# Kernel optimization log

Measured on AMD Instinct MI355X. Metric: run time of the kernel, lower is better.

## Reference

```python
import jax, jax.numpy as jnp
import numpy as np

# Constants from TensorBase init_kwargs
AABB_MIN, AABB_MAX = -1.5, 1.5
NEAR, FAR = 2.0, 6.0
DENSITY_SHIFT = -10.0
DISTANCE_SCALE = 25.0
VIEW_PE, FEA_PE = 6, 6


def positional_encoding(x, freqs):
    # matches torch positional_encoding: interleave over freq axis, then sin/cos concat
    fb = 2.0 ** jnp.arange(freqs, dtype=x.dtype)  # [F]
    pts = (x[..., None] * fb).reshape(x.shape[:-1] + (freqs * x.shape[-1],))
    return jnp.concatenate([jnp.sin(pts), jnp.cos(pts)], axis=-1)


def trilinear_sample(vol, coords):
    """Emulates F.grid_sample(vol[None], coords, align_corners=True, padding_mode='zeros').
    vol: [C, D, H, W]; coords: [M, 3] xyz in [-1, 1] (x->W, y->H, z->D). Returns [M, C]."""
    C, D, H, W = vol.shape
    in_bounds = jnp.all((coords >= -1.0) & (coords <= 1.0), axis=-1)  # [M]
    x = jnp.clip((coords[:, 0] + 1.0) * 0.5 * (W - 1), 0.0, W - 1)
    y = jnp.clip((coords[:, 1] + 1.0) * 0.5 * (H - 1), 0.0, H - 1)
    z = jnp.clip((coords[:, 2] + 1.0) * 0.5 * (D - 1), 0.0, D - 1)
    x0 = jnp.clip(jnp.floor(x).astype(jnp.int32), 0, W - 2); x1 = x0 + 1
    y0 = jnp.clip(jnp.floor(y).astype(jnp.int32), 0, H - 2); y1 = y0 + 1
    z0 = jnp.clip(jnp.floor(z).astype(jnp.int32), 0, D - 2); z1 = z0 + 1
    fx = (x - x0)[None]; fy = (y - y0)[None]; fz = (z - z0)[None]  # [1,M]
    g = lambda zi, yi, xi: vol[:, zi, yi, xi]  # [C, M] gather
    c00 = g(z0, y0, x0) * (1 - fx) + g(z0, y0, x1) * fx
    c01 = g(z0, y1, x0) * (1 - fx) + g(z0, y1, x1) * fx
    c10 = g(z1, y0, x0) * (1 - fx) + g(z1, y0, x1) * fx
    c11 = g(z1, y1, x0) * (1 - fx) + g(z1, y1, x1) * fx
    c0 = c00 * (1 - fy) + c01 * fy
    c1 = c10 * (1 - fy) + c11 * fy
    out = c0 * (1 - fz) + c1 * fz  # [C, M]
    return (out * in_bounds[None].astype(vol.dtype)).T  # [M, C]


def setup_inputs() -> dict:
    key = jax.random.key(0)
    ks = jax.random.split(key, 10)
    N, G, APP_DIM, FC = 2048, 128, 27, 128
    in_mlpC = 2 * VIEW_PE * 3 + 2 * FEA_PE * APP_DIM + 3 + APP_DIM  # 390
    return {
        "rays_o": jax.random.normal(ks[0], (N, 3), jnp.float32) * 0.1,
        "rays_d": jax.random.normal(ks[1], (N, 3), jnp.float32),
        "density_grid": jax.random.normal(ks[2], (1, G, G, G), jnp.float32),
        "app_grid": jax.random.normal(ks[3], (APP_DIM, G, G, G), jnp.float32) * 0.1,
        "W1": jax.random.normal(ks[4], (in_mlpC, FC), jnp.float32) * (1.0 / np.sqrt(in_mlpC)),
        "b1": jnp.zeros((FC,), jnp.float32),
        "W2": jax.random.normal(ks[5], (FC, FC), jnp.float32) * (1.0 / np.sqrt(FC)),
        "b2": jnp.zeros((FC,), jnp.float32),
        "W3": jax.random.normal(ks[6], (FC, 3), jnp.float32) * (1.0 / np.sqrt(FC)),
        "b3": jnp.zeros((3,), jnp.float32),
        "n_samples": 128,
    }


def reference(rays_o, rays_d, density_grid, app_grid, W1, b1, W2, b2, W3, b3, n_samples):
    N = rays_o.shape[0]
    S = int(n_samples)
    dirs = rays_d / jnp.linalg.norm(rays_d, axis=-1, keepdims=True)
    # sample points along rays: [N, S, 3]
    t = jnp.linspace(NEAR, FAR, S, dtype=rays_o.dtype)
    pts = rays_o[:, None, :] + dirs[:, None, :] * t[None, :, None]
    # normalize_coord: (xyz - aabb[0]) * invaabbSize - 1
    norm_pts = (pts - AABB_MIN) * (2.0 / (AABB_MAX - AABB_MIN)) - 1.0
    flat = norm_pts.reshape(-1, 3)  # [N*S, 3]
    # density feature lookup + feature2density (softplus with density_shift)
    sigma_feat = trilinear_sample(density_grid, flat)[:, 0].reshape(N, S)
    sigma = jax.nn.softplus(sigma_feat + DENSITY_SHIFT)
    # raw2alpha with cumprod transmittance
    delta = (FAR - NEAR) / S
    alpha = 1.0 - jnp.exp(-sigma * delta * DISTANCE_SCALE)  # [N, S]
    T = jnp.cumprod(jnp.concatenate([jnp.ones((N, 1), alpha.dtype), 1.0 - alpha + 1e-10], axis=-1), axis=-1)
    weights = alpha * T[:, :-1]  # [N, S]
    acc = jnp.sum(weights, axis=-1)  # [N]
    # appearance feature lookup + MLPRender_Fea shading
    feats = trilinear_sample(app_grid, flat)  # [N*S, 27]
    vd = jnp.broadcast_to(dirs[:, None, :], (N, S, 3)).reshape(-1, 3)
    mlp_in = jnp.concatenate([feats, vd, positional_encoding(feats, FEA_PE), positional_encoding(vd, VIEW_PE)], axis=-1)
    h = jax.nn.relu(mlp_in @ W1 + b1)
    h = jax.nn.relu(h @ W2 + b2)
    rgb = jax.nn.sigmoid(h @ W3 + b3).reshape(N, S, 3)
    # composite with white background
    rgb_map = jnp.sum(weights[..., None] * rgb, axis=1) + (1.0 - acc)[:, None]
    return jnp.clip(rgb_map, 0.0, 1.0)
```

## Files before the change

kernel.cpp:

```cpp
#include <hip/hip_runtime.h>

#define NRAYS 2048
#define NS    128
#define G     128
#define FC    128
#define APPC  27
#define TILE  8
#define MAXP  48
#define R1    351

static __device__ __forceinline__ float tri_sample(const float* __restrict__ vol,
                                                   float gx, float gy, float gz) {
  int x0 = (int)gx; x0 = x0 < 0 ? 0 : (x0 > G - 2 ? G - 2 : x0);
  int y0 = (int)gy; y0 = y0 < 0 ? 0 : (y0 > G - 2 ? G - 2 : y0);
  int z0 = (int)gz; z0 = z0 < 0 ? 0 : (z0 > G - 2 ? G - 2 : z0);
  float fx = gx - (float)x0;
  float fy = gy - (float)y0;
  float fz = gz - (float)z0;
  const float* p = vol + ((z0 * G + y0) * G + x0);
  float v000 = p[0], v001 = p[1];
  float v010 = p[G], v011 = p[G + 1];
  const float* q = p + G * G;
  float v100 = q[0], v101 = q[1];
  float v110 = q[G], v111 = q[G + 1];
  float c00 = v000 + (v001 - v000) * fx;
  float c01 = v010 + (v011 - v010) * fx;
  float c10 = v100 + (v101 - v100) * fx;
  float c11 = v110 + (v111 - v110) * fx;
  float c0  = c00 + (c01 - c00) * fy;
  float c1  = c10 + (c11 - c10) * fy;
  return c0 + (c1 - c0) * fz;
}

static __device__ __forceinline__ float sample_alpha(const float* __restrict__ dgrid,
                                                     float ox, float oy, float oz,
                                                     float dx, float dy, float dz,
                                                     int s, bool& inb) {
  const float t  = 2.0f + (4.0f / 127.0f) * (float)s;
  const float px = (ox + dx * t) * (2.0f / 3.0f);
  const float py = (oy + dy * t) * (2.0f / 3.0f);
  const float pz = (oz + dz * t) * (2.0f / 3.0f);
  inb = (fabsf(px) <= 1.0f) && (fabsf(py) <= 1.0f) && (fabsf(pz) <= 1.0f);
  float sf = 0.0f;
  if (inb)
    sf = tri_sample(dgrid, (px + 1.0f) * 63.5f, (py + 1.0f) * 63.5f, (pz + 1.0f) * 63.5f);
  const float y  = __expf(sf - 10.0f);
  const float sp = y - 0.5f * y * y;
  return 1.0f - __expf(-sp * 0.78125f);
}

__global__ __launch_bounds__(256) void k_phase1(
    const float* __restrict__ rays_o, const float* __restrict__ rays_d,
    const float* __restrict__ dgrid,
    const float* __restrict__ W1, const float* __restrict__ W2,
    const float* __restrict__ W3, const float* __restrict__ b1,
    const float* __restrict__ b2, const float* __restrict__ b3,
    float* __restrict__ out, float* __restrict__ g_dir,
    float* __restrict__ g_woob, float* __restrict__ g_hbase,
    float* __restrict__ g_rgboob, unsigned char* __restrict__ g_cnt8,
    unsigned char* __restrict__ g_sidx, float* __restrict__ g_w) {
  const int bid = blockIdx.x;
  const int tid = threadIdx.x;

  if (bid < 512) {
    const int ray  = bid * 4 + (tid >> 6);
    const int lane = tid & 63;

    const float rdx = rays_d[ray * 3 + 0], rdy = rays_d[ray * 3 + 1], rdz = rays_d[ray * 3 + 2];
    const float inv = rsqrtf(rdx * rdx + rdy * rdy + rdz * rdz);
    const float dx = rdx * inv, dy = rdy * inv, dz = rdz * inv;
    const float ox = rays_o[ray * 3 + 0], oy = rays_o[ray * 3 + 1], oz = rays_o[ray * 3 + 2];
    if (lane == 0) {
      g_dir[ray * 3 + 0] = dx; g_dir[ray * 3 + 1] = dy; g_dir[ray * 3 + 2] = dz;
    }

    const int s0 = lane * 2, s1 = s0 + 1;
    bool in0, in1;
    const float al0 = sample_alpha(dgrid, ox, oy, oz, dx, dy, dz, s0, in0);
    const float al1 = sample_alpha(dgrid, ox, oy, oz, dx, dy, dz, s1, in1);

    const float p0 = 1.0f - al0 + 1e-10f;
    const float p1 = 1.0f - al1 + 1e-10f;
    float incl = p0 * p1;
#pragma unroll
    for (int off = 1; off < 64; off <<= 1) {
      float v = __shfl_up(incl, off);
      if (lane >= off) incl *= v;
    }
    float excl = __shfl_up(incl, 1);
    if (lane == 0) excl = 1.0f;
    const float w0 = al0 * excl;
    const float w1 = al1 * excl * p0;

    float acc  = w0 + w1;
    float woob = (in0 ? 0.0f : w0) + (in1 ? 0.0f : w1);
#pragma unroll
    for (int off = 32; off > 0; off >>= 1) {
      acc  += __shfl_xor(acc, off);
      woob += __shfl_xor(woob, off);
    }

    const unsigned long long m0 = __ballot(in0);
    const unsigned long long m1 = __ballot(in1);
    const int n_in = (int)__popcll(m0) + (int)__popcll(m1);

    if (lane == 0) {
      g_woob[ray] = woob;
      g_cnt8[ray] = (unsigned char)((n_in > MAXP) ? MAXP : n_in);
    }
    if (lane < 3) out[ray * 3 + lane] = 1.0f - acc;

    const unsigned long long low = (1ull << lane) - 1ull;
    const int r0 = (int)__popcll(m0 & low) + (int)__popcll(m1 & low);
    if (in0 && r0 < MAXP) {
      g_sidx[ray * MAXP + r0] = (unsigned char)s0;
      g_w[ray * MAXP + r0]    = w0;
    }
    if (in1) {
      const int r1 = r0 + (in0 ? 1 : 0);
      if (r1 < MAXP) {
        g_sidx[ray * MAXP + r1] = (unsigned char)s1;
        g_w[ray * MAXP + r1]    = w1;
      }
    }
    return;
  }

  __shared__ float s_in[39][8];
  __shared__ float s_h1[FC][12];
  __shared__ float s_h2[FC][12];
  __shared__ float s_bc[FC], s_ps[FC];

  const int r0 = (bid - 512) * 8;
  if (tid < 24) {
    const int j = tid & 7, d = tid >> 3;
    const float rdx = rays_d[(r0 + j) * 3 + 0], rdy = rays_d[(r0 + j) * 3 + 1],
                rdz = rays_d[(r0 + j) * 3 + 2];
    const float inv = rsqrtf(rdx * rdx + rdy * rdy + rdz * rdz);
    s_in[d][j] = (d == 0) ? rdx * inv : ((d == 1) ? rdy * inv : rdz * inv);
  }
  {
    const int nrn = tid & 127, h = tid >> 7;
    float v = 0.0f;
#pragma unroll 9
    for (int k = 192 + h; k < 354; k += 2) v += W1[k * FC + nrn];
    if (h) s_ps[nrn] = v; else s_bc[nrn] = v;
  }
  __syncthreads();
  for (int a = tid; a < 18 * 8; a += 256) {
    const int j = a & 7, idx = a >> 3, d = idx / 6, f = idx % 6;
    float sn, cs; __sincosf(s_in[d][j] * (float)(1 << f), &sn, &cs);
    s_in[3 + idx][j]  = sn;
    s_in[21 + idx][j] = cs;
  }
  __syncthreads();

  const int nrn = tid & 127;
  const int j0  = (tid >> 7) * 4;

  float a1[4];
  {
    const float bb = b1[nrn];
#pragma unroll
    for (int i = 0; i < 4; ++i) a1[i] = bb;
  }
#pragma unroll
  for (int r = 0; r < 39; ++r) {
    const int k = (r < 3) ? (27 + r) : (351 + r);
    const float wv = W1[k * FC + nrn];
    const float4 v0 = *(const float4*)&s_in[r][j0];
    a1[0] = fmaf(v0.x, wv, a1[0]); a1[1] = fmaf(v0.y, wv, a1[1]);
    a1[2] = fmaf(v0.z, wv, a1[2]); a1[3] = fmaf(v0.w, wv, a1[3]);
  }
  const float bcv = s_bc[nrn] + s_ps[nrn];
#pragma unroll
  for (int i = 0; i < 4; ++i) {
    g_hbase[(size_t)(r0 + j0 + i) * FC + nrn] = a1[i];
    s_h1[nrn][j0 + i] = fmaxf(a1[i] + bcv, 0.0f);
  }
  __syncthreads();

  float a2[4];
  {
    const float bb = b2[nrn];
#pragma unroll
    for (int i = 0; i < 4; ++i) a2[i] = bb;
  }
#pragma unroll 4
  for (int k = 0; k < FC; ++k) {
    const float wv = W2[k * FC + nrn];
    const float4 u0 = *(const float4*)&s_h1[k][j0];
    a2[0] = fmaf(u0.x, wv, a2[0]); a2[1] = fmaf(u0.y, wv, a2[1]);
    a2[2] = fmaf(u0.z, wv, a2[2]); a2[3] = fmaf(u0.w, wv, a2[3]);
  }
#pragma unroll
  for (int i = 0; i < 4; ++i) s_h2[nrn][j0 + i] = fmaxf(a2[i], 0.0f);
  __syncthreads();

  if (tid < 24) {
    const int j = tid / 3, c = tid - j * 3;
    float a3 = b3[c];
#pragma unroll 8
    for (int k = 0; k < FC; ++k)
      a3 = fmaf(s_h2[k][j], W3[k * 3 + c], a3);
    g_rgboob[(r0 + j) * 3 + c] = 1.0f / (1.0f + __expf(-a3));
  }
}

__global__ __launch_bounds__(256) void k_items(const float* __restrict__ rays_o,
                                               const float* __restrict__ g_dir,
                                               const float* __restrict__ agrid,
                                               const float* __restrict__ W1,
                                               const float* __restrict__ W2,
                                               const float* __restrict__ W3,
                                               const float* __restrict__ b2,
                                               const float* __restrict__ b3,
                                               const float* __restrict__ g_hbase,
                                               const float* __restrict__ g_woob,
                                               const float* __restrict__ g_rgboob,
                                               const unsigned char* __restrict__ g_cnt8,
                                               const unsigned char* __restrict__ g_sidx,
                                               const float* __restrict__ g_w,
                                               float* __restrict__ out) {
  const int tid = threadIdx.x;
  __shared__ int   s_pfx[NRAYS + 1];
  __shared__ int   s_wt[4];
  __shared__ float s_inT[R1][TILE];
  __shared__ float s_hT[FC][12];
  __shared__ int   s_rayid[TILE];
  __shared__ float s_jw[TILE], s_gx[TILE], s_gy[TILE], s_gz[TILE];
  __shared__ int   s_vld[TILE];

  {
    const int b0 = tid * 8;
    const uint2 cc = *(const uint2*)&g_cnt8[b0];
    int c8[8];
#pragma unroll
    for (int i = 0; i < 4; ++i) c8[i]     = (int)((cc.x >> (8 * i)) & 0xff);
#pragma unroll
    for (int i = 0; i < 4; ++i) c8[4 + i] = (int)((cc.y >> (8 * i)) & 0xff);
    int ex[8], run = 0;
#pragma unroll
    for (int i = 0; i < 8; ++i) { ex[i] = run; run += c8[i]; }
    int inclv = run;
    const int lane = tid & 63;
#pragma unroll
    for (int off = 1; off < 64; off <<= 1) {
      int v = __shfl_up(inclv, off);
      if (lane >= off) inclv += v;
    }
    if (lane == 63) s_wt[tid >> 6] = inclv;
    __syncthreads();
    int woff = 0;
    const int wq = tid >> 6;
    if (wq > 0) woff += s_wt[0];
    if (wq > 1) woff += s_wt[1];
    if (wq > 2) woff += s_wt[2];
    const int tbase = woff + inclv - run;
#pragma unroll
    for (int i = 0; i < 8; ++i) s_pfx[b0 + i] = tbase + ex[i];
    if (tid == 255) s_pfx[NRAYS] = tbase + run;
  }
  __syncthreads();
  const int total  = s_pfx[NRAYS];
  const int ntiles = 8 + ((total + TILE - 1) >> 3);

  for (int tile = blockIdx.x; tile < ntiles; tile += gridDim.x) {
    if (tile < 8) {
      const int ray = tile * 256 + tid;
      const float wv = g_woob[ray];
#pragma unroll
      for (int c = 0; c < 3; ++c)
        atomicAdd(&out[ray * 3 + c], wv * g_rgboob[ray * 3 + c]);
      continue;
    }
    const int it = tile - 8;

    if (tid < TILE) {
      const int gi  = it * TILE + tid;
      const int vld = gi < total;
      int ray = 0, s = 0;
      float wj = 0.0f;
      if (vld) {
        int lo = 0, hi = NRAYS - 1;
        while (lo < hi) {
          const int mid = (lo + hi + 1) >> 1;
          if (s_pfx[mid] <= gi) lo = mid; else hi = mid - 1;
        }
        ray = lo;
        const int slot = gi - s_pfx[ray];
        s  = g_sidx[ray * MAXP + slot];
        wj = g_w[ray * MAXP + slot];
      }
      s_rayid[tid] = ray;
      s_vld[tid]   = vld;
      s_jw[tid]    = wj;
      const float dxx = g_dir[ray * 3 + 0], dyy = g_dir[ray * 3 + 1], dzz = g_dir[ray * 3 + 2];
      const float t = 2.0f + (4.0f / 127.0f) * (float)s;
      s_gx[tid] = ((rays_o[ray * 3 + 0] + dxx * t) * (2.0f / 3.0f) + 1.0f) * 63.5f;
      s_gy[tid] = ((rays_o[ray * 3 + 1] + dyy * t) * (2.0f / 3.0f) + 1.0f) * 63.5f;
      s_gz[tid] = ((rays_o[ray * 3 + 2] + dzz * t) * (2.0f / 3.0f) + 1.0f) * 63.5f;
    }
    __syncthreads();

    if (tid < APPC * TILE) {
      const int j = tid & (TILE - 1), c = tid >> 3;
      s_inT[c][j] = s_vld[j]
                        ? tri_sample(agrid + (size_t)c * G * G * G, s_gx[j], s_gy[j], s_gz[j])
                        : 0.0f;
    }
    __syncthreads();

    for (int a = tid; a < 162 * TILE; a += 256) {
      const int j = a & (TILE - 1), idx = a >> 3;
      const int d = idx / 6, f = idx % 6;
      float sn, cs; __sincosf(s_inT[d][j] * (float)(1 << f), &sn, &cs);
      s_inT[27 + idx][j]  = sn;
      s_inT[189 + idx][j] = cs;
    }
    __syncthreads();

    const int nrn = tid & 127;
    const int j0  = (tid >> 7) * 4;

    float a1[4];
#pragma unroll
    for (int i = 0; i < 4; ++i)
      a1[i] = g_hbase[(size_t)s_rayid[j0 + i] * FC + nrn];

    const float* w1p = W1 + nrn;
#pragma unroll 9
    for (int r = 0; r < 27; ++r) {
      const float wv = w1p[r * FC];
      const float4 v0 = *(const float4*)&s_inT[r][j0];
      a1[0] = fmaf(v0.x, wv, a1[0]); a1[1] = fmaf(v0.y, wv, a1[1]);
      a1[2] = fmaf(v0.z, wv, a1[2]); a1[3] = fmaf(v0.w, wv, a1[3]);
    }
#pragma unroll 8
    for (int r = 27; r < R1; ++r) {
      const float wv = w1p[(r + 3) * FC];
      const float4 v0 = *(const float4*)&s_inT[r][j0];
      a1[0] = fmaf(v0.x, wv, a1[0]); a1[1] = fmaf(v0.y, wv, a1[1]);
      a1[2] = fmaf(v0.z, wv, a1[2]); a1[3] = fmaf(v0.w, wv, a1[3]);
    }
#pragma unroll
    for (int i = 0; i < 4; ++i) s_hT[nrn][j0 + i] = fmaxf(a1[i], 0.0f);
    __syncthreads();

    float a2[4];
    {
      const float bb = b2[nrn];
#pragma unroll
      for (int i = 0; i < 4; ++i) a2[i] = bb;
    }
#pragma unroll 4
    for (int k = 0; k < FC; ++k) {
      const float wv = W2[k * FC + nrn];
      const float4 u0 = *(const float4*)&s_hT[k][j0];
      a2[0] = fmaf(u0.x, wv, a2[0]); a2[1] = fmaf(u0.y, wv, a2[1]);
      a2[2] = fmaf(u0.z, wv, a2[2]); a2[3] = fmaf(u0.w, wv, a2[3]);
    }
    float* s_h2 = &s_inT[0][0];
#pragma unroll
    for (int i = 0; i < 4; ++i) s_h2[nrn * 12 + j0 + i] = fmaxf(a2[i], 0.0f);
    __syncthreads();

    if (tid < 3 * TILE) {
      const int j = tid / 3, c = tid - j * 3;
      if (s_vld[j] && s_jw[j] != 0.0f) {
        float a3 = b3[c];
#pragma unroll 8
        for (int k = 0; k < FC; ++k)
          a3 = fmaf(s_h2[k * 12 + j], W3[k * 3 + c], a3);
        const float rgb = 1.0f / (1.0f + __expf(-a3));
        atomicAdd(&out[s_rayid[j] * 3 + c], s_jw[j] * rgb);
      }
    }
    __syncthreads();
  }
}

extern "C" void kernel_launch(void* const* d_in, const int* in_sizes, int n_in,
                              void* d_out, int out_size, void* d_ws, size_t ws_size,
                              hipStream_t stream) {
  const float* rays_o = (const float*)d_in[0];
  const float* rays_d = (const float*)d_in[1];
  const float* dgrid  = (const float*)d_in[2];
  const float* agrid  = (const float*)d_in[3];
  const float* W1     = (const float*)d_in[4];
  const float* b1     = (const float*)d_in[5];
  const float* W2     = (const float*)d_in[6];
  const float* b2     = (const float*)d_in[7];
  const float* W3     = (const float*)d_in[8];
  const float* b3     = (const float*)d_in[9];
  float* out = (float*)d_out;

  char* ws = (char*)d_ws;
  float*         g_dir    = (float*)(ws);
  float*         g_woob   = (float*)(ws + 24576);
  float*         g_rgboob = (float*)(ws + 32768);
  unsigned char* g_cnt8   = (unsigned char*)(ws + 57344);
  float*         g_hbase  = (float*)(ws + 65536);
  float*         g_w      = (float*)(ws + 65536 + 1048576);
  unsigned char* g_sidx   = (unsigned char*)(ws + 65536 + 1048576 + 393216);

  hipLaunchKernelGGL(k_phase1, dim3(768), dim3(256), 0, stream,
                     rays_o, rays_d, dgrid, W1, W2, W3, b1, b2, b3,
                     out, g_dir, g_woob, g_hbase, g_rgboob, g_cnt8, g_sidx, g_w);
  hipLaunchKernelGGL(k_items, dim3(768), dim3(256), 0, stream,
                     rays_o, g_dir, agrid, W1, W2, W3, b2, b3,
                     g_hbase, g_woob, g_rgboob, g_cnt8, g_sidx, g_w, out);
}
```

Baseline: 58.98 us.

## Fuse out-of-bounds MLP into density kernel and drop precomputed hidden base

The density/transmittance pass now also runs the out-of-bounds MLP for its 4 rays in the same block and writes the background-plus-OOB colour directly, removing the separate OOB blocks and the atomicAdd tile loop. The item kernel no longer reads a per-ray precomputed layer-1 base from global memory. Instead it recomputes the direction and its positional encoding in idle threads and runs the full 390-row first layer. This trades 39 extra FMA rows per item and some shared memory for less global traffic, no atomics and a smaller workspace. The MLP in the prep kernel is split across two half-blocks with shared-memory reductions.

```diff
diff --git a/kernel.cpp b/kernel.cpp
--- a/kernel.cpp
+++ b/kernel.cpp
@@ -7,7 +7,7 @@
 #define APPC  27
 #define TILE  8
 #define MAXP  48
-#define R1    351
+#define NB2   768
 
 static __device__ __forceinline__ float tri_sample(const float* __restrict__ vol,
                                                    float gx, float gy, float gz) {
@@ -49,22 +49,31 @@
   return 1.0f - __expf(-sp * 0.78125f);
 }
 
-__global__ __launch_bounds__(256) void k_phase1(
+__global__ __launch_bounds__(256) void k_prep(
     const float* __restrict__ rays_o, const float* __restrict__ rays_d,
     const float* __restrict__ dgrid,
     const float* __restrict__ W1, const float* __restrict__ W2,
     const float* __restrict__ W3, const float* __restrict__ b1,
     const float* __restrict__ b2, const float* __restrict__ b3,
     float* __restrict__ out, float* __restrict__ g_dir,
-    float* __restrict__ g_woob, float* __restrict__ g_hbase,
-    float* __restrict__ g_rgboob, unsigned char* __restrict__ g_cnt8,
+    unsigned char* __restrict__ g_cnt8,
     unsigned char* __restrict__ g_sidx, float* __restrict__ g_w) {
   const int bid = blockIdx.x;
   const int tid = threadIdx.x;
 
-  if (bid < 512) {
-    const int ray  = bid * 4 + (tid >> 6);
+  __shared__ float s_dir[3][4];
+  __shared__ float s_woob[4], s_acc[4];
+  __shared__ float s_bc[FC], s_ps[FC];
+  __shared__ float s_in[39][4];
+  __shared__ float s_p[2][FC][4];
+  __shared__ float s_h1[FC][4];
+  __shared__ float s_h2[FC][4];
+  __shared__ float s_p3[12][2];
+
+  {
+    const int w    = tid >> 6;
     const int lane = tid & 63;
+    const int ray  = bid * 4 + w;
 
     const float rdx = rays_d[ray * 3 + 0], rdy = rays_d[ray * 3 + 1], rdz = rays_d[ray * 3 + 2];
     const float inv = rsqrtf(rdx * rdx + rdy * rdy + rdz * rdz);
@@ -72,6 +81,7 @@
     const float ox = rays_o[ray * 3 + 0], oy = rays_o[ray * 3 + 1], oz = rays_o[ray * 3 + 2];
     if (lane == 0) {
       g_dir[ray * 3 + 0] = dx; g_dir[ray * 3 + 1] = dy; g_dir[ray * 3 + 2] = dz;
+      s_dir[0][w] = dx; s_dir[1][w] = dy; s_dir[2][w] = dz;
     }
 
     const int s0 = lane * 2, s1 = s0 + 1;
@@ -105,10 +115,10 @@
     const int n_in = (int)__popcll(m0) + (int)__popcll(m1);
 
     if (lane == 0) {
-      g_woob[ray] = woob;
+      s_woob[w] = woob;
+      s_acc[w]  = acc;
       g_cnt8[ray] = (unsigned char)((n_in > MAXP) ? MAXP : n_in);
     }
-    if (lane < 3) out[ray * 3 + lane] = 1.0f - acc;
 
     const unsigned long long low = (1ull << lane) - 1ull;
     const int r0 = (int)__popcll(m0 & low) + (int)__popcll(m1 & low);
@@ -123,22 +133,8 @@
         g_w[ray * MAXP + r1]    = w1;
       }
     }
-    return;
-  }
-
-  __shared__ float s_in[39][8];
-  __shared__ float s_h1[FC][12];
-  __shared__ float s_h2[FC][12];
-  __shared__ float s_bc[FC], s_ps[FC];
-
-  const int r0 = (bid - 512) * 8;
-  if (tid < 24) {
-    const int j = tid & 7, d = tid >> 3;
-    const float rdx = rays_d[(r0 + j) * 3 + 0], rdy = rays_d[(r0 + j) * 3 + 1],
-                rdz = rays_d[(r0 + j) * 3 + 2];
-    const float inv = rsqrtf(rdx * rdx + rdy * rdy + rdz * rdz);
-    s_in[d][j] = (d == 0) ? rdx * inv : ((d == 1) ? rdy * inv : rdz * inv);
-  }
+  }
+
   {
     const int nrn = tid & 127, h = tid >> 7;
     float v = 0.0f;
@@ -147,63 +143,92 @@
     if (h) s_ps[nrn] = v; else s_bc[nrn] = v;
   }
   __syncthreads();
-  for (int a = tid; a < 18 * 8; a += 256) {
-    const int j = a & 7, idx = a >> 3, d = idx / 6, f = idx % 6;
-    float sn, cs; __sincosf(s_in[d][j] * (float)(1 << f), &sn, &cs);
+
+  if (tid < 12) {
+    const int j = tid & 3, d = tid >> 2;
+    s_in[d][j] = s_dir[d][j];
+  }
+  for (int a = tid; a < 72; a += 256) {
+    const int j = a & 3, idx = a >> 2, d = idx / 6, f = idx % 6;
+    float sn, cs; __sincosf(s_dir[d][j] * (float)(1 << f), &sn, &cs);
     s_in[3 + idx][j]  = sn;
     s_in[21 + idx][j] = cs;
   }
   __syncthreads();
 
   const int nrn = tid & 127;
-  const int j0  = (tid >> 7) * 4;
-
-  float a1[4];
+  const int h   = tid >> 7;
+
   {
-    const float bb = b1[nrn];
-#pragma unroll
-    for (int i = 0; i < 4; ++i) a1[i] = bb;
-  }
-#pragma unroll
-  for (int r = 0; r < 39; ++r) {
-    const int k = (r < 3) ? (27 + r) : (351 + r);
-    const float wv = W1[k * FC + nrn];
-    const float4 v0 = *(const float4*)&s_in[r][j0];
-    a1[0] = fmaf(v0.x, wv, a1[0]); a1[1] = fmaf(v0.y, wv, a1[1]);
-    a1[2] = fmaf(v0.z, wv, a1[2]); a1[3] = fmaf(v0.w, wv, a1[3]);
-  }
-  const float bcv = s_bc[nrn] + s_ps[nrn];
-#pragma unroll
-  for (int i = 0; i < 4; ++i) {
-    g_hbase[(size_t)(r0 + j0 + i) * FC + nrn] = a1[i];
-    s_h1[nrn][j0 + i] = fmaxf(a1[i] + bcv, 0.0f);
-  }
-  __syncthreads();
-
-  float a2[4];
+    float a1[4];
+    const float init = h ? (s_bc[nrn] + s_ps[nrn]) : b1[nrn];
+#pragma unroll
+    for (int i = 0; i < 4; ++i) a1[i] = h ? init : init;
+#pragma unroll
+    for (int i = 0; i < 4; ++i) a1[i] = init;
+    const int rlo = h ? 20 : 0, rhi = h ? 39 : 20;
+    for (int r = rlo; r < rhi; ++r) {
+      const int k = (r < 3) ? (27 + r) : (351 + r);
+      const float wv = W1[k * FC + nrn];
+      const float4 v0 = *(const float4*)&s_in[r][0];
+      a1[0] = fmaf(v0.x, wv, a1[0]); a1[1] = fmaf(v0.y, wv, a1[1]);
+      a1[2] = fmaf(v0.z, wv, a1[2]); a1[3] = fmaf(v0.w, wv, a1[3]);
+    }
+    *(float4*)&s_p[h][nrn][0] = make_float4(a1[0], a1[1], a1[2], a1[3]);
+  }
+  __syncthreads();
+  if (tid < FC) {
+    const float4 q0 = *(const float4*)&s_p[0][tid][0];
+    const float4 q1 = *(const float4*)&s_p[1][tid][0];
+    s_h1[tid][0] = fmaxf(q0.x + q1.x, 0.0f);
+    s_h1[tid][1] = fmaxf(q0.y + q1.y, 0.0f);
+    s_h1[tid][2] = fmaxf(q0.z + q1.z, 0.0f);
+    s_h1[tid][3] = fmaxf(q0.w + q1.w, 0.0f);
+  }
+  __syncthreads();
+
   {
-    const float bb = b2[nrn];
-#pragma unroll
-    for (int i = 0; i < 4; ++i) a2[i] = bb;
-  }
+    float a2[4] = {0.0f, 0.0f, 0.0f, 0.0f};
+    const int k0 = h * 64;
 #pragma unroll 4
-  for (int k = 0; k < FC; ++k) {
-    const float wv = W2[k * FC + nrn];
-    const float4 u0 = *(const float4*)&s_h1[k][j0];
-    a2[0] = fmaf(u0.x, wv, a2[0]); a2[1] = fmaf(u0.y, wv, a2[1]);
-    a2[2] = fmaf(u0.z, wv, a2[2]); a2[3] = fmaf(u0.w, wv, a2[3]);
-  }
-#pragma unroll
-  for (int i = 0; i < 4; ++i) s_h2[nrn][j0 + i] = fmaxf(a2[i], 0.0f);
+    for (int kk = 0; kk < 64; ++kk) {
+      const int k = k0 + kk;
+      const float wv = W2[k * FC + nrn];
+      const float4 u0 = *(const float4*)&s_h1[k][0];
+      a2[0] = fmaf(u0.x, wv, a2[0]); a2[1] = fmaf(u0.y, wv, a2[1]);
+      a2[2] = fmaf(u0.z, wv, a2[2]); a2[3] = fmaf(u0.w, wv, a2[3]);
+    }
+    *(float4*)&s_p[h][nrn][0] = make_float4(a2[0], a2[1], a2[2], a2[3]);
+  }
+  __syncthreads();
+  if (tid < FC) {
+    const float bb = b2[tid];
+    const float4 q0 = *(const float4*)&s_p[0][tid][0];
+    const float4 q1 = *(const float4*)&s_p[1][tid][0];
+    s_h2[tid][0] = fmaxf(bb + q0.x + q1.x, 0.0f);
+    s_h2[tid][1] = fmaxf(bb + q0.y + q1.y, 0.0f);
+    s_h2[tid][2] = fmaxf(bb + q0.z + q1.z, 0.0f);
+    s_h2[tid][3] = fmaxf(bb + q0.w + q1.w, 0.0f);
+  }
   __syncthreads();
 
   if (tid < 24) {
+    const int q = tid >> 1, hf = tid & 1;
+    const int j = q / 3, c = q - j * 3;
+    float a3 = 0.0f;
+#pragma unroll 8
+    for (int kk = 0; kk < 64; ++kk) {
+      const int k = hf * 64 + kk;
+      a3 = fmaf(s_h2[k][j], W3[k * 3 + c], a3);
+    }
+    s_p3[q][hf] = a3;
+  }
+  __syncthreads();
+  if (tid < 12) {
     const int j = tid / 3, c = tid - j * 3;
-    float a3 = b3[c];
-#pragma unroll 8
-    for (int k = 0; k < FC; ++k)
-      a3 = fmaf(s_h2[k][j], W3[k * 3 + c], a3);
-    g_rgboob[(r0 + j) * 3 + c] = 1.0f / (1.0f + __expf(-a3));
+    const float a3  = b3[c] + s_p3[tid][0] + s_p3[tid][1];
+    const float rgb = 1.0f / (1.0f + __expf(-a3));
+    out[(bid * 4 + j) * 3 + c] = s_woob[j] * rgb + (1.0f - s_acc[j]);
   }
 }
 
@@ -213,11 +238,9 @@
                                                const float* __restrict__ W1,
                                                const float* __restrict__ W2,
                                                const float* __restrict__ W3,
+                                               const float* __restrict__ b1,
                                                const float* __restrict__ b2,
                                                const float* __restrict__ b3,
-                                               const float* __restrict__ g_hbase,
-                                               const float* __restrict__ g_woob,
-                                               const float* __restrict__ g_rgboob,
                                                const unsigned char* __restrict__ g_cnt8,
                                                const unsigned char* __restrict__ g_sidx,
                                                const float* __restrict__ g_w,
@@ -225,7 +248,7 @@
   const int tid = threadIdx.x;
   __shared__ int   s_pfx[NRAYS + 1];
   __shared__ int   s_wt[4];
-  __shared__ float s_inT[R1][TILE];
+  __shared__ float s_inT[390][TILE];
   __shared__ float s_hT[FC][12];
   __shared__ int   s_rayid[TILE];
   __shared__ float s_jw[TILE], s_gx[TILE], s_gy[TILE], s_gz[TILE];
@@ -263,21 +286,11 @@
   }
   __syncthreads();
   const int total  = s_pfx[NRAYS];
-  const int ntiles = 8 + ((total + TILE - 1) >> 3);
-
-  for (int tile = blockIdx.x; tile < ntiles; tile += gridDim.x) {
-    if (tile < 8) {
-      const int ray = tile * 256 + tid;
-      const float wv = g_woob[ray];
-#pragma unroll
-      for (int c = 0; c < 3; ++c)
-        atomicAdd(&out[ray * 3 + c], wv * g_rgboob[ray * 3 + c]);
-      continue;
-    }
-    const int it = tile - 8;
-
+  const int ntiles = (total + TILE - 1) >> 3;
+
+  for (int tile = blockIdx.x; tile < ntiles; tile += NB2) {
     if (tid < TILE) {
-      const int gi  = it * TILE + tid;
+      const int gi  = tile * TILE + tid;
       const int vld = gi < total;
       int ray = 0, s = 0;
       float wj = 0.0f;
@@ -308,6 +321,19 @@
       s_inT[c][j] = s_vld[j]
                         ? tri_sample(agrid + (size_t)c * G * G * G, s_gx[j], s_gy[j], s_gz[j])
                         : 0.0f;
+    } else {
+      for (int a = tid - 216; a < 24; a += 40) {
+        const int j = a & 7, d = a >> 3;
+        s_inT[351 + d][j] = g_dir[s_rayid[j] * 3 + d];
+      }
+      for (int a = tid - 216; a < 144; a += 40) {
+        const int j = a & 7, idx = a >> 3;
+        const int d = idx / 6, f = idx % 6;
+        const float dv = g_dir[s_rayid[j] * 3 + d];
+        float sn, cs; __sincosf(dv * (float)(1 << f), &sn, &cs);
+        s_inT[354 + idx][j] = sn;
+        s_inT[372 + idx][j] = cs;
+      }
     }
     __syncthreads();
 
@@ -324,10 +350,11 @@
     const int j0  = (tid >> 7) * 4;
 
     float a1[4];
-#pragma unroll
-    for (int i = 0; i < 4; ++i)
-      a1[i] = g_hbase[(size_t)s_rayid[j0 + i] * FC + nrn];
-
+    {
+      const float bb = b1[nrn];
+#pragma unroll
+      for (int i = 0; i < 4; ++i) a1[i] = bb;
+    }
     const float* w1p = W1 + nrn;
 #pragma unroll 9
     for (int r = 0; r < 27; ++r) {
@@ -337,8 +364,16 @@
       a1[2] = fmaf(v0.z, wv, a1[2]); a1[3] = fmaf(v0.w, wv, a1[3]);
     }
 #pragma unroll 8
-    for (int r = 27; r < R1; ++r) {
+    for (int r = 27; r < 351; ++r) {
       const float wv = w1p[(r + 3) * FC];
+      const float4 v0 = *(const float4*)&s_inT[r][j0];
+      a1[0] = fmaf(v0.x, wv, a1[0]); a1[1] = fmaf(v0.y, wv, a1[1]);
+      a1[2] = fmaf(v0.z, wv, a1[2]); a1[3] = fmaf(v0.w, wv, a1[3]);
+    }
+#pragma unroll
+    for (int r = 351; r < 390; ++r) {
+      const int k = (r < 354) ? (r - 324) : r;
+      const float wv = w1p[k * FC];
       const float4 v0 = *(const float4*)&s_inT[r][j0];
       a1[0] = fmaf(v0.x, wv, a1[0]); a1[1] = fmaf(v0.y, wv, a1[1]);
       a1[2] = fmaf(v0.z, wv, a1[2]); a1[3] = fmaf(v0.w, wv, a1[3]);
@@ -396,18 +431,15 @@
   float* out = (float*)d_out;
 
   char* ws = (char*)d_ws;
-  float*         g_dir    = (float*)(ws);
-  float*         g_woob   = (float*)(ws + 24576);
-  float*         g_rgboob = (float*)(ws + 32768);
-  unsigned char* g_cnt8   = (unsigned char*)(ws + 57344);
-  float*         g_hbase  = (float*)(ws + 65536);
-  float*         g_w      = (float*)(ws + 65536 + 1048576);
-  unsigned char* g_sidx   = (unsigned char*)(ws + 65536 + 1048576 + 393216);
-
-  hipLaunchKernelGGL(k_phase1, dim3(768), dim3(256), 0, stream,
+  float*         g_dir  = (float*)(ws);
+  unsigned char* g_cnt8 = (unsigned char*)(ws + 24576);
+  float*         g_w    = (float*)(ws + 32768);
+  unsigned char* g_sidx = (unsigned char*)(ws + 32768 + 393216);
+
+  hipLaunchKernelGGL(k_prep, dim3(NRAYS / 4), dim3(256), 0, stream,
                      rays_o, rays_d, dgrid, W1, W2, W3, b1, b2, b3,
-                     out, g_dir, g_woob, g_hbase, g_rgboob, g_cnt8, g_sidx, g_w);
-  hipLaunchKernelGGL(k_items, dim3(768), dim3(256), 0, stream,
-                     rays_o, g_dir, agrid, W1, W2, W3, b2, b3,
-                     g_hbase, g_woob, g_rgboob, g_cnt8, g_sidx, g_w, out);
+                     out, g_dir, g_cnt8, g_sidx, g_w);
+  hipLaunchKernelGGL(k_items, dim3(NB2), dim3(256), 0, stream,
+                     rays_o, g_dir, agrid, W1, W2, W3, b1, b2, b3,
+                     g_cnt8, g_sidx, g_w, out);
 }
```

Result: slower. 66.00 us (+11.9%).
